# Kernel tuning notes

Hardware: AMD Instinct MI355X
Metric: run time of the kernel (lower is better)

## Reference

```python
import jax, jax.numpy as jnp
import numpy as np

T, B, D, H, L = 512, 512, 64, 128, 2
Y_LEN = 24


def gru_cell(x, h, Wih, Whh, bih, bhh):
    # PyTorch GRU cell, gate order (r, z, n)
    gi = x @ Wih.T + bih          # [B, 3H]
    gh = h @ Whh.T + bhh          # [B, 3H]
    ir, iz, i_n = jnp.split(gi, 3, axis=-1)
    hr, hz, h_n = jnp.split(gh, 3, axis=-1)
    r = jax.nn.sigmoid(ir + hr)
    z = jax.nn.sigmoid(iz + hz)
    n = jnp.tanh(i_n + r * h_n)
    return (1.0 - z) * n + z * h


def bigru_layer(inp, h0, Wih, Whh, bih, bhh):
    # inp [T,B,in]; Wih [2,3H,in]; Whh [2,3H,H]; bih/bhh [2,3H]; h0 [2,B,H]
    def step_f(h, x):
        h = gru_cell(x, h, Wih[0], Whh[0], bih[0], bhh[0])
        return h, h

    def step_b(h, x):
        h = gru_cell(x, h, Wih[1], Whh[1], bih[1], bhh[1])
        return h, h

    hf, out_f = jax.lax.scan(step_f, h0[0], inp)
    hb, out_b = jax.lax.scan(step_b, h0[1], jnp.flip(inp, 0))
    out_b = jnp.flip(out_b, 0)
    return jnp.concatenate([out_f, out_b], -1), hf, hb


def forward(x, enc_Wih0, enc_Wih1, enc_Whh, enc_bih, enc_bhh,
            dec_Wih0, dec_Wih1, dec_Whh, dec_bih, dec_bhh, fc_w, fc_b):
    batch = x.shape[1]
    # ---- encoder: 2-layer bidirectional GRU, h0 = 0 ----
    layer_in = x
    hn = []
    for l in range(L):
        Wih = enc_Wih0 if l == 0 else enc_Wih1
        h0 = jnp.zeros((2, batch, H), x.dtype)
        layer_in, hf, hb = bigru_layer(layer_in, h0, Wih, enc_Whh[l], enc_bih[l], enc_bhh[l])
        hn += [hf, hb]
    dec_h = jnp.stack(hn)                # [2L, B, H], layer-major (fwd, bwd)
    # dropout on h0 is eval-mode identity
    x0 = x[-1, :, 0:1]                   # [B, 1]

    def step(carry, _):
        xin, h = carry
        lin = xin
        new_h = []
        for l in range(L):
            Wih = dec_Wih0 if l == 0 else dec_Wih1
            hf = gru_cell(lin, h[2 * l],     Wih[0], dec_Whh[l, 0], dec_bih[l, 0], dec_bhh[l, 0])
            hb = gru_cell(lin, h[2 * l + 1], Wih[1], dec_Whh[l, 1], dec_bih[l, 1], dec_bhh[l, 1])
            lin = jnp.concatenate([hf, hb], -1)
            new_h += [hf, hb]
        pred = lin @ fc_w.T + fc_b       # [B, 1]
        return (pred, jnp.stack(new_h)), pred[:, 0]

    _, preds = jax.lax.scan(step, (x0, dec_h), None, length=Y_LEN)
    return preds[..., None]              # [24, B, 1]


def setup_inputs():
    key = jax.random.key(0)
    ks = jax.random.split(key, 13)
    scale = 1.0 / np.sqrt(H).astype(np.float32)
    u = lambda k, shape: jax.random.uniform(k, shape, jnp.float32, -scale, scale)
    return {
        "x": jax.random.normal(ks[0], (T, B, D), jnp.float32),
        "enc_Wih0": u(ks[1], (2, 3 * H, D)),
        "enc_Wih1": u(ks[2], (2, 3 * H, 2 * H)),
        "enc_Whh": u(ks[3], (L, 2, 3 * H, H)),
        "enc_bih": u(ks[4], (L, 2, 3 * H)),
        "enc_bhh": u(ks[5], (L, 2, 3 * H)),
        "dec_Wih0": u(ks[6], (2, 3 * H, 1)),
        "dec_Wih1": u(ks[7], (2, 3 * H, 2 * H)),
        "dec_Whh": u(ks[8], (L, 2, 3 * H, H)),
        "dec_bih": u(ks[9], (L, 2, 3 * H)),
        "dec_bhh": u(ks[10], (L, 2, 3 * H)),
        "fc_w": u(ks[11], (1, 2 * H)),
        "fc_b": u(ks[12], (1,)),
    }


def reference(x, enc_Wih0, enc_Wih1, enc_Whh, enc_bih, enc_bhh,
              dec_Wih0, dec_Wih1, dec_Whh, dec_bih, dec_bhh, fc_w, fc_b):
    return forward(x, enc_Wih0, enc_Wih1, enc_Whh, enc_bih, enc_bhh,
                   dec_Wih0, dec_Wih1, dec_Whh, dec_bih, dec_bhh, fc_w, fc_b)
```

## Files before the change

### kernel.cpp

```cpp
#include <hip/hip_runtime.h>
#include <cstdint>
#include <cstddef>


typedef __attribute__((ext_vector_type(8))) short short8_t;
typedef __attribute__((ext_vector_type(4))) short short4_t;
typedef __attribute__((ext_vector_type(4))) float f32x4_t;

#define MFMA16(a, b, c) __builtin_amdgcn_mfma_f32_16x16x32_bf16((a), (b), (c), 0, 0, 0)

static __device__ __forceinline__ float bf2f(unsigned short u) {
  unsigned int v = ((unsigned int)u) << 16;
  return __builtin_bit_cast(float, v);
}
static __device__ __forceinline__ unsigned short f2bf(float f) {
  unsigned int x = __builtin_bit_cast(unsigned int, f);
  x += 0x7fffu + ((x >> 16) & 1u);
  return (unsigned short)(x >> 16);
}
static __device__ __forceinline__ short8_t ld8(const unsigned short* p) {
  return *reinterpret_cast<const short8_t*>(p);
}
static __device__ __forceinline__ short8_t cvt8f(const float* p) {
  const f32x4_t* v = reinterpret_cast<const f32x4_t*>(p);
  f32x4_t a = v[0], b = v[1];
  short8_t r;
  r[0] = (short)f2bf(a[0]); r[1] = (short)f2bf(a[1]);
  r[2] = (short)f2bf(a[2]); r[3] = (short)f2bf(a[3]);
  r[4] = (short)f2bf(b[0]); r[5] = (short)f2bf(b[1]);
  r[6] = (short)f2bf(b[2]); r[7] = (short)f2bf(b[3]);
  return r;
}
static __device__ __forceinline__ float sigm(float x) { return 1.0f / (1.0f + __expf(-x)); }
static __device__ __forceinline__ float tanh_fast(float y) {
  float t = __expf(-2.0f * fabsf(y));
  float r = (1.0f - t) / (1.0f + t);
  return copysignf(r, y);
}

__global__ void k_prep(const float* __restrict__ x,
                       const float* __restrict__ dWih1, const float* __restrict__ dWhh,
                       unsigned short* __restrict__ bdWih1, unsigned short* __restrict__ bdWhh,
                       float* __restrict__ x0save) {
  const int NW = 24576;
  int i = blockIdx.x * blockDim.x + threadIdx.x;
  if (i < NW) {
    *reinterpret_cast<short8_t*>(bdWih1 + (size_t)i * 8) = cvt8f(dWih1 + (size_t)i * 8);
  } else if (i < 2 * NW) {
    int j = i - NW;
    *reinterpret_cast<short8_t*>(bdWhh + (size_t)j * 8) = cvt8f(dWhh + (size_t)j * 8);
  } else if (i < 2 * NW + 512) {
    int b = i - 2 * NW;
    x0save[b] = x[((size_t)511 * 512 + b) * 64];
  }
}

__global__ void k_copy(const float* __restrict__ x, float* __restrict__ xc,
                       int b_base, int Bc) {
  size_t i = (size_t)blockIdx.x * blockDim.x + threadIdx.x;
  size_t per = (size_t)Bc * 16;
  size_t n = (size_t)512 * per;
  if (i >= n) return;
  size_t t = i / per, r = i - t * per;
  const f32x4_t* s =
      reinterpret_cast<const f32x4_t*>(x + ((size_t)t * 512 + b_base) * 64) + r;
  f32x4_t* d = reinterpret_cast<f32x4_t*>(xc + t * per * 4) + r;
  *d = *s;
}

__global__ __launch_bounds__(256, 1) void k_scan0d(
    float* x,
    float* xc,
    const float* __restrict__ Wih,
    const float* __restrict__ bih,
    const float* __restrict__ Whh,
    const float* __restrict__ bhh,
    float* __restrict__ HS,
    int b_base, int Bc) {
  int dir = blockIdx.y;
  int bl0 = blockIdx.x * 16;
  int b0g = b_base + bl0;
  float* xin = dir ? xc : x;
  unsigned short* yout = (unsigned short*)xin;
  int xstr = dir ? Bc : 512;
  int xb0 = dir ? bl0 : b0g;
  int tid = threadIdx.x, w = tid >> 6, lane = tid & 63, q = lane >> 4, c16 = lane & 15;
  __shared__ unsigned short xl[2][16 * 72];
  __shared__ unsigned short hl[2][16 * 136];
  const float* Wi = Wih + (size_t)dir * 384 * 64;
  const float* Wh = Whh + (size_t)dir * 384 * 128;
  const float* bi = bih + dir * 384;
  const float* bh = bhh + dir * 384;

  short8_t fi[6][2], fh[6][4];
  float brz[4], bni[2], bnh[2];
#pragma unroll
  for (int g = 0; g < 3; g++)
#pragma unroll
    for (int cc = 0; cc < 2; cc++) {
      int f = g * 2 + cc;
      int n0 = g * 128 + w * 32 + cc * 16;
#pragma unroll
      for (int kt = 0; kt < 2; kt++)
        fi[f][kt] = cvt8f(Wi + (size_t)(n0 + c16) * 64 + kt * 32 + q * 8);
#pragma unroll
      for (int kt = 0; kt < 4; kt++)
        fh[f][kt] = cvt8f(Wh + (size_t)(n0 + c16) * 128 + kt * 32 + q * 8);
      if (g < 2) brz[f] = bi[n0 + c16] + bh[n0 + c16];
      else { bni[cc] = bi[n0 + c16]; bnh[cc] = bh[n0 + c16]; }
    }

  float h[2][4];
#pragma unroll
  for (int cc = 0; cc < 2; cc++)
#pragma unroll
    for (int rr = 0; rr < 4; rr++) h[cc][rr] = 0.f;
  for (int i = tid; i < 16 * 136; i += 256) hl[0][i] = 0;

  int srow = tid >> 4, sc = tid & 15;
  {
    int t0 = dir ? 511 : 0;
    f32x4_t v = *reinterpret_cast<const f32x4_t*>(
        xin + ((size_t)t0 * xstr + xb0 + srow) * 64 + sc * 4);
    unsigned short* dst = &xl[0][srow * 72 + sc * 4];
    dst[0] = f2bf(v[0]); dst[1] = f2bf(v[1]); dst[2] = f2bf(v[2]); dst[3] = f2bf(v[3]);
  }
  __syncthreads();

  for (int s = 0; s < 512; s++) {
    int cur = s & 1, nxt = cur ^ 1;
    if (s > 0) {
      int tp = dir ? (512 - s) : (s - 1);
      short8_t v = ld8(&hl[cur][srow * 136 + sc * 8]);
      *reinterpret_cast<short8_t*>(
          yout + ((size_t)tp * xstr + xb0 + srow) * 128 + sc * 8) = v;
    }
    f32x4_t xv;
    if (s < 511) {
      int tn = dir ? (510 - s) : (s + 1);
      xv = *reinterpret_cast<const f32x4_t*>(
          xin + ((size_t)tn * xstr + xb0 + srow) * 64 + sc * 4);
    }
    short8_t ax[2], ah[4];
#pragma unroll
    for (int kt = 0; kt < 2; kt++) ax[kt] = ld8(&xl[cur][c16 * 72 + kt * 32 + q * 8]);
#pragma unroll
    for (int kt = 0; kt < 4; kt++) ah[kt] = ld8(&hl[cur][c16 * 136 + kt * 32 + q * 8]);
    f32x4_t aRZ[4], aNi[2], aNh[2];
#pragma unroll
    for (int f = 0; f < 4; f++) aRZ[f] = (f32x4_t){0.f, 0.f, 0.f, 0.f};
#pragma unroll
    for (int cc = 0; cc < 2; cc++) {
      aNi[cc] = (f32x4_t){0.f, 0.f, 0.f, 0.f};
      aNh[cc] = (f32x4_t){0.f, 0.f, 0.f, 0.f};
    }
#pragma unroll
    for (int kt = 0; kt < 2; kt++) {
#pragma unroll
      for (int f = 0; f < 4; f++) aRZ[f] = MFMA16(ax[kt], fi[f][kt], aRZ[f]);
#pragma unroll
      for (int cc = 0; cc < 2; cc++) aNi[cc] = MFMA16(ax[kt], fi[4 + cc][kt], aNi[cc]);
    }
#pragma unroll
    for (int kt = 0; kt < 4; kt++) {
#pragma unroll
      for (int f = 0; f < 4; f++) aRZ[f] = MFMA16(ah[kt], fh[f][kt], aRZ[f]);
#pragma unroll
      for (int cc = 0; cc < 2; cc++) aNh[cc] = MFMA16(ah[kt], fh[4 + cc][kt], aNh[cc]);
    }
#pragma unroll
    for (int cc = 0; cc < 2; cc++)
#pragma unroll
      for (int rr = 0; rr < 4; rr++) {
        float r = sigm(aRZ[cc][rr] + brz[cc]);
        float z = sigm(aRZ[2 + cc][rr] + brz[2 + cc]);
        float n = tanh_fast(aNi[cc][rr] + bni[cc] + r * (aNh[cc][rr] + bnh[cc]));
        float hn = n + z * (h[cc][rr] - n);
        h[cc][rr] = hn;
        hl[nxt][(q * 4 + rr) * 136 + w * 32 + c16 + cc * 16] = f2bf(hn);
      }
    if (s < 511) {
      unsigned short* dst = &xl[nxt][srow * 72 + sc * 4];
      dst[0] = f2bf(xv[0]); dst[1] = f2bf(xv[1]); dst[2] = f2bf(xv[2]); dst[3] = f2bf(xv[3]);
    }
    __syncthreads();
  }
  {
    int tp = dir ? 0 : 511;
    short8_t v = ld8(&hl[0][srow * 136 + sc * 8]);
    *reinterpret_cast<short8_t*>(
        yout + ((size_t)tp * xstr + xb0 + srow) * 128 + sc * 8) = v;
  }
#pragma unroll
  for (int cc = 0; cc < 2; cc++)
#pragma unroll
    for (int rr = 0; rr < 4; rr++)
      HS[((size_t)dir * 512 + b0g + q * 4 + rr) * 128 + w * 32 + c16 + cc * 16] = h[cc][rr];
}

__global__ __launch_bounds__(512, 1) void k_scan1(
    const unsigned short* __restrict__ OutF,
    const unsigned short* __restrict__ OutB,
    const float* __restrict__ Wih1,
    const float* __restrict__ bih1,
    const float* __restrict__ Whh1,
    const float* __restrict__ bhh1,
    float* __restrict__ HS,
    int b_base, int Bc) {
  int dir = blockIdx.y;
  int b0l = blockIdx.x * 16;
  int tid = threadIdx.x, w = tid >> 6, lane = tid & 63, q = lane >> 4, c16 = lane & 15;
  __shared__ unsigned short il[2][16 * 264];
  __shared__ unsigned short hl[2][16 * 136];
  const float* Wi = Wih1 + (size_t)dir * 384 * 256;
  const float* Wh = Whh1 + (size_t)dir * 384 * 128;
  const float* bi = bih1 + dir * 384;
  const float* bh = bhh1 + dir * 384;

  short8_t fi[3][8], fh[3][4];
  float brz[2], bni, bnh;
#pragma unroll
  for (int g = 0; g < 3; g++) {
    int n0 = g * 128 + w * 16;
#pragma unroll
    for (int kt = 0; kt < 8; kt++)
      fi[g][kt] = cvt8f(Wi + (size_t)(n0 + c16) * 256 + kt * 32 + q * 8);
#pragma unroll
    for (int kt = 0; kt < 4; kt++)
      fh[g][kt] = cvt8f(Wh + (size_t)(n0 + c16) * 128 + kt * 32 + q * 8);
    if (g < 2) brz[g] = bi[n0 + c16] + bh[n0 + c16];
    else { bni = bi[n0 + c16]; bnh = bh[n0 + c16]; }
  }

  float h[4] = {0.f, 0.f, 0.f, 0.f};
  for (int i = tid; i < 16 * 136; i += 512) hl[0][i] = 0;

  int srow = tid >> 5, sc = tid & 31;
  {
    int t0 = dir ? 511 : 0;
    short8_t v = (sc < 16)
        ? ld8(OutF + ((size_t)t0 * 512 + b_base + b0l + srow) * 128 + sc * 8)
        : ld8(OutB + ((size_t)t0 * Bc + b0l + srow) * 128 + (sc - 16) * 8);
    *reinterpret_cast<short8_t*>(&il[0][srow * 264 + sc * 8]) = v;
  }
  __syncthreads();

  for (int s = 0; s < 512; s++) {
    int cur = s & 1, nxt = cur ^ 1;
    short8_t iv;
    if (s < 511) {
      int tn = dir ? (510 - s) : (s + 1);
      iv = (sc < 16)
          ? ld8(OutF + ((size_t)tn * 512 + b_base + b0l + srow) * 128 + sc * 8)
          : ld8(OutB + ((size_t)tn * Bc + b0l + srow) * 128 + (sc - 16) * 8);
    }
    f32x4_t aI[3], aH[3];
#pragma unroll
    for (int g = 0; g < 3; g++) {
      aI[g] = (f32x4_t){0.f, 0.f, 0.f, 0.f};
      aH[g] = (f32x4_t){0.f, 0.f, 0.f, 0.f};
    }
#pragma unroll
    for (int kt = 0; kt < 8; kt++) {
      short8_t a = ld8(&il[cur][c16 * 264 + kt * 32 + q * 8]);
#pragma unroll
      for (int g = 0; g < 3; g++) aI[g] = MFMA16(a, fi[g][kt], aI[g]);
    }
#pragma unroll
    for (int kt = 0; kt < 4; kt++) {
      short8_t a = ld8(&hl[cur][c16 * 136 + kt * 32 + q * 8]);
#pragma unroll
      for (int g = 0; g < 3; g++) aH[g] = MFMA16(a, fh[g][kt], aH[g]);
    }
#pragma unroll
    for (int rr = 0; rr < 4; rr++) {
      float r = sigm(aI[0][rr] + aH[0][rr] + brz[0]);
      float z = sigm(aI[1][rr] + aH[1][rr] + brz[1]);
      float n = tanh_fast(aI[2][rr] + bni + r * (aH[2][rr] + bnh));
      float hn = n + z * (h[rr] - n);
      h[rr] = hn;
      hl[nxt][(q * 4 + rr) * 136 + w * 16 + c16] = f2bf(hn);
    }
    if (s < 511)
      *reinterpret_cast<short8_t*>(&il[nxt][srow * 264 + sc * 8]) = iv;
    __syncthreads();
  }
#pragma unroll
  for (int rr = 0; rr < 4; rr++)
    HS[((size_t)(2 + dir) * 512 + b_base + b0l + q * 4 + rr) * 128 + w * 16 + c16] = h[rr];
}

__global__ __launch_bounds__(512, 1) void k_dec(
    const float* __restrict__ x0save,
    const float* __restrict__ HS,
    const unsigned short* __restrict__ Whh,
    const unsigned short* __restrict__ Wih1,
    const float* __restrict__ Wih0,
    const float* __restrict__ bih,
    const float* __restrict__ bhh,
    const float* __restrict__ fc_w,
    const float* __restrict__ fcb,
    float* __restrict__ out) {
  int b0 = blockIdx.x * 16;
  int tid = threadIdx.x, w = tid >> 6, lane = tid & 63, q = lane >> 4, c16 = lane & 15;
  int d = w >> 2, w4 = w & 3;
  __shared__ unsigned short hc0[16 * 264];
  __shared__ unsigned short hc1[16 * 264];
  __shared__ float x0s[16];
  __shared__ float fcwf[256];
  int jj = w4 * 32 + c16;
  int jw = w4 * 32;

  const unsigned short* Wd0 = Whh + (size_t)d * 384 * 128;
  const unsigned short* Wh1 = Whh + (size_t)(2 + d) * 384 * 128;
  const unsigned short* Wi1 = Wih1 + (size_t)d * 384 * 256;

  float hs[2][2][4];
#pragma unroll
  for (int l = 0; l < 2; l++)
#pragma unroll
    for (int cc = 0; cc < 2; cc++)
#pragma unroll
      for (int rr = 0; rr < 4; rr++) {
        int row = q * 4 + rr, j = jj + cc * 16;
        int cell = l * 2 + d;
        float v = HS[((size_t)cell * 512 + b0 + row) * 128 + j];
        hs[l][cc][rr] = v;
        unsigned short bv = f2bf(v);
        unsigned short* tile = l ? hc1 : hc0;
        tile[row * 264 + d * 128 + j] = bv;
      }
  if (tid < 16) x0s[tid] = x0save[b0 + tid];
  if (tid < 256) fcwf[tid] = fc_w[tid];

  float w0c[2][3], bi0[2][3], bh0[2][3], bi1[2][3], bh1[2][3];
#pragma unroll
  for (int cc = 0; cc < 2; cc++)
#pragma unroll
    for (int g = 0; g < 3; g++) {
      int col = g * 128 + jj + cc * 16;
      w0c[cc][g] = Wih0[d * 384 + col];
      bi0[cc][g] = bih[d * 384 + col];
      bh0[cc][g] = bhh[d * 384 + col];
      bi1[cc][g] = bih[(2 + d) * 384 + col];
      bh1[cc][g] = bhh[(2 + d) * 384 + col];
    }
  __syncthreads();

  for (int st = 0; st < 24; st++) {
    float hn0[2][4];
    {
      short8_t a0[4];
#pragma unroll
      for (int kt = 0; kt < 4; kt++)
        a0[kt] = ld8(&hc0[c16 * 264 + d * 128 + kt * 32 + q * 8]);
      short8_t w0[24];
#pragma unroll
      for (int kt = 0; kt < 4; kt++)
#pragma unroll
        for (int g = 0; g < 3; g++)
#pragma unroll
          for (int cc = 0; cc < 2; cc++) {
            int n0 = g * 128 + jw + cc * 16;
            w0[kt * 6 + g * 2 + cc] =
                ld8(Wd0 + (size_t)(n0 + c16) * 128 + kt * 32 + q * 8);
          }
      f32x4_t acc[6];
#pragma unroll
      for (int f = 0; f < 6; f++) acc[f] = (f32x4_t){0.f, 0.f, 0.f, 0.f};
#pragma unroll
      for (int kt = 0; kt < 4; kt++)
#pragma unroll
        for (int g = 0; g < 3; g++)
#pragma unroll
          for (int cc = 0; cc < 2; cc++) {
            int f = g * 2 + cc;
            acc[f] = MFMA16(a0[kt], w0[kt * 6 + g * 2 + cc], acc[f]);
          }
#pragma unroll
      for (int cc = 0; cc < 2; cc++)
#pragma unroll
        for (int rr = 0; rr < 4; rr++) {
          float xin = x0s[q * 4 + rr];
          float r = sigm(xin * w0c[cc][0] + bi0[cc][0] + acc[cc][rr] + bh0[cc][0]);
          float z = sigm(xin * w0c[cc][1] + bi0[cc][1] + acc[2 + cc][rr] + bh0[cc][1]);
          float n = tanh_fast(xin * w0c[cc][2] + bi0[cc][2] +
                              r * (acc[4 + cc][rr] + bh0[cc][2]));
          float hv = n + z * (hs[0][cc][rr] - n);
          hn0[cc][rr] = hv;
          hs[0][cc][rr] = hv;
        }
    }
    __syncthreads();
#pragma unroll
    for (int cc = 0; cc < 2; cc++)
#pragma unroll
      for (int rr = 0; rr < 4; rr++)
        hc0[(q * 4 + rr) * 264 + d * 128 + jj + cc * 16] = f2bf(hn0[cc][rr]);
    __syncthreads();

    float hn1[2][4];
    {
      short8_t ai[8];
#pragma unroll
      for (int kt = 0; kt < 8; kt++) ai[kt] = ld8(&hc0[c16 * 264 + kt * 32 + q * 8]);
      short8_t ah[4];
#pragma unroll
      for (int kt = 0; kt < 4; kt++)
        ah[kt] = ld8(&hc1[c16 * 264 + d * 128 + kt * 32 + q * 8]);
      f32x4_t aRZ[4], aNi[2], aNh[2];
#pragma unroll
      for (int f = 0; f < 4; f++) aRZ[f] = (f32x4_t){0.f, 0.f, 0.f, 0.f};
#pragma unroll
      for (int cc = 0; cc < 2; cc++) {
        aNi[cc] = (f32x4_t){0.f, 0.f, 0.f, 0.f};
        aNh[cc] = (f32x4_t){0.f, 0.f, 0.f, 0.f};
      }
      {
        short8_t wA[24];
#pragma unroll
        for (int kt = 0; kt < 4; kt++) {
#pragma unroll
          for (int f = 0; f < 4; f++) {
            int n0 = (f >> 1) * 128 + jw + (f & 1) * 16;
            wA[kt * 6 + f] = ld8(Wi1 + (size_t)(n0 + c16) * 256 + kt * 32 + q * 8);
          }
#pragma unroll
          for (int cc = 0; cc < 2; cc++) {
            int n0 = 256 + jw + cc * 16;
            wA[kt * 6 + 4 + cc] = ld8(Wi1 + (size_t)(n0 + c16) * 256 + kt * 32 + q * 8);
          }
        }
#pragma unroll
        for (int kt = 0; kt < 4; kt++) {
#pragma unroll
          for (int f = 0; f < 4; f++) aRZ[f] = MFMA16(ai[kt], wA[kt * 6 + f], aRZ[f]);
#pragma unroll
          for (int cc = 0; cc < 2; cc++) aNi[cc] = MFMA16(ai[kt], wA[kt * 6 + 4 + cc], aNi[cc]);
        }
      }
      {
        short8_t wB[24];
#pragma unroll
        for (int kt = 0; kt < 4; kt++) {
#pragma unroll
          for (int f = 0; f < 4; f++) {
            int n0 = (f >> 1) * 128 + jw + (f & 1) * 16;
            wB[kt * 6 + f] = ld8(Wi1 + (size_t)(n0 + c16) * 256 + (kt + 4) * 32 + q * 8);
          }
#pragma unroll
          for (int cc = 0; cc < 2; cc++) {
            int n0 = 256 + jw + cc * 16;
            wB[kt * 6 + 4 + cc] = ld8(Wi1 + (size_t)(n0 + c16) * 256 + (kt + 4) * 32 + q * 8);
          }
        }
#pragma unroll
        for (int kt = 0; kt < 4; kt++) {
#pragma unroll
          for (int f = 0; f < 4; f++) aRZ[f] = MFMA16(ai[4 + kt], wB[kt * 6 + f], aRZ[f]);
#pragma unroll
          for (int cc = 0; cc < 2; cc++) aNi[cc] = MFMA16(ai[4 + kt], wB[kt * 6 + 4 + cc], aNi[cc]);
        }
      }
      {
        short8_t wH[24];
#pragma unroll
        for (int kt = 0; kt < 4; kt++) {
#pragma unroll
          for (int f = 0; f < 4; f++) {
            int n0 = (f >> 1) * 128 + jw + (f & 1) * 16;
            wH[kt * 6 + f] = ld8(Wh1 + (size_t)(n0 + c16) * 128 + kt * 32 + q * 8);
          }
#pragma unroll
          for (int cc = 0; cc < 2; cc++) {
            int n0 = 256 + jw + cc * 16;
            wH[kt * 6 + 4 + cc] = ld8(Wh1 + (size_t)(n0 + c16) * 128 + kt * 32 + q * 8);
          }
        }
#pragma unroll
        for (int kt = 0; kt < 4; kt++) {
#pragma unroll
          for (int f = 0; f < 4; f++) aRZ[f] = MFMA16(ah[kt], wH[kt * 6 + f], aRZ[f]);
#pragma unroll
          for (int cc = 0; cc < 2; cc++) aNh[cc] = MFMA16(ah[kt], wH[kt * 6 + 4 + cc], aNh[cc]);
        }
      }
#pragma unroll
      for (int cc = 0; cc < 2; cc++)
#pragma unroll
        for (int rr = 0; rr < 4; rr++) {
          float r = sigm(aRZ[cc][rr] + bi1[cc][0] + bh1[cc][0]);
          float z = sigm(aRZ[2 + cc][rr] + bi1[cc][1] + bh1[cc][1]);
          float n = tanh_fast(aNi[cc][rr] + bi1[cc][2] + r * (aNh[cc][rr] + bh1[cc][2]));
          float hv = n + z * (hs[1][cc][rr] - n);
          hn1[cc][rr] = hv;
          hs[1][cc][rr] = hv;
        }
    }
    __syncthreads();
#pragma unroll
    for (int cc = 0; cc < 2; cc++)
#pragma unroll
      for (int rr = 0; rr < 4; rr++)
        hc1[(q * 4 + rr) * 264 + d * 128 + jj + cc * 16] = f2bf(hn1[cc][rr]);
    __syncthreads();

    if (w == 0) {
      float s = 0.f;
#pragma unroll
      for (int i = 0; i < 8; i++) {
        short8_t hv = ld8(&hc1[c16 * 264 + q * 64 + i * 8]);
#pragma unroll
        for (int e = 0; e < 8; e++)
          s += bf2f((unsigned short)hv[e]) * fcwf[q * 64 + i * 8 + e];
      }
      s += __shfl_xor(s, 16);
      s += __shfl_xor(s, 32);
      if (q == 0) {
        float pred = s + fcb[0];
        x0s[c16] = pred;
        out[(size_t)st * 512 + b0 + c16] = pred;
      }
    }
    __syncthreads();
  }
}

extern "C" void kernel_launch(void* const* d_in, const int* in_sizes, int n_in,
                              void* d_out, int out_size, void* d_ws, size_t ws_size,
                              hipStream_t stream) {
  const float* x     = (const float*)d_in[0];
  const float* eWih0 = (const float*)d_in[1];
  const float* eWih1 = (const float*)d_in[2];
  const float* eWhh  = (const float*)d_in[3];
  const float* ebih  = (const float*)d_in[4];
  const float* ebhh  = (const float*)d_in[5];
  const float* dWih0 = (const float*)d_in[6];
  const float* dWih1 = (const float*)d_in[7];
  const float* dWhh  = (const float*)d_in[8];
  const float* dbih  = (const float*)d_in[9];
  const float* dbhh  = (const float*)d_in[10];
  const float* fc_w  = (const float*)d_in[11];
  const float* fc_b  = (const float*)d_in[12];
  float* out = (float*)d_out;
  (void)in_sizes; (void)n_in; (void)out_size;

  const size_t fixedB = 2048 + 1048576 + 393216 + 393216 + 4096;
  int Bc = 256;
  if (fixedB + (size_t)512 * 131072 <= ws_size) Bc = 512;

  char* ws = (char*)d_ws;
  size_t off = 0;
  auto alloc = [&](size_t bytes) -> char* {
    off = (off + 255) & ~(size_t)255;
    char* p = ws + off;
    off += bytes;
    return p;
  };
  float* x0save          = (float*)alloc(2048);
  float* HS              = (float*)alloc(1048576);
  unsigned short* bdWih1 = (unsigned short*)alloc(393216);
  unsigned short* bdWhh  = (unsigned short*)alloc(393216);
  float* xc              = (float*)alloc((size_t)Bc * 131072);

  k_prep<<<194, 256, 0, stream>>>(x, dWih1, dWhh, bdWih1, bdWhh, x0save);

  float* xm = (float*)d_in[0];
  const float* Whh1 = eWhh + (size_t)2 * 384 * 128;
  int nchunks = 512 / Bc;
  for (int c = 0; c < nchunks; c++) {
    int b_base = c * Bc;
    int ncopy = (512 * Bc * 16 + 255) / 256;
    k_copy<<<ncopy, 256, 0, stream>>>(x, xc, b_base, Bc);
    k_scan0d<<<dim3(Bc / 16, 2), 256, 0, stream>>>(xm, xc, eWih0, ebih, eWhh, ebhh,
                                                   HS, b_base, Bc);
    k_scan1<<<dim3(Bc / 16, 2), 512, 0, stream>>>((const unsigned short*)xm,
                                                  (const unsigned short*)xc,
                                                  eWih1, ebih + 768, Whh1,
                                                  ebhh + 768, HS, b_base, Bc);
  }
  k_dec<<<dim3(32), 512, 0, stream>>>(x0save, HS, bdWhh, bdWih1, dWih0, dbih, dbhh,
                                      fc_w, fc_b, out);
}
```

Measured before the change: 2.083 ms.

## Prefetch scan inputs two steps ahead and use LDS-only barrier

Both encoder scan kernels now issue the global load for the input two timesteps ahead, keeping it in registers that alternate between two buffers via a manually unrolled loop of two steps. The per-step __syncthreads is replaced with an inline-asm barrier that waits only on LDS counters, so the outstanding global prefetch no longer has to finish at each barrier. This is meant to hide global load latency on the serial recurrence critical path. The cost is extra registers, plus reliance on the asm barrier being correct for the ordering of the global y-output stores.

```diff
diff --git a/kernel.cpp b/kernel.cpp
--- a/kernel.cpp
+++ b/kernel.cpp
@@ -8,6 +8,8 @@
 typedef __attribute__((ext_vector_type(4))) float f32x4_t;
 
 #define MFMA16(a, b, c) __builtin_amdgcn_mfma_f32_16x16x32_bf16((a), (b), (c), 0, 0, 0)
+
+#define BAR_LDS() asm volatile("s_waitcnt lgkmcnt(0)\n\ts_barrier" ::: "memory")
 
 static __device__ __forceinline__ float bf2f(unsigned short u) {
   unsigned int v = ((unsigned int)u) << 16;
@@ -20,6 +22,9 @@
 }
 static __device__ __forceinline__ short8_t ld8(const unsigned short* p) {
   return *reinterpret_cast<const short8_t*>(p);
+}
+static __device__ __forceinline__ f32x4_t ldf4(const float* p) {
+  return *reinterpret_cast<const f32x4_t*>(p);
 }
 static __device__ __forceinline__ short8_t cvt8f(const float* p) {
   const f32x4_t* v = reinterpret_cast<const f32x4_t*>(p);
@@ -120,26 +125,28 @@
   int srow = tid >> 4, sc = tid & 15;
   {
     int t0 = dir ? 511 : 0;
-    f32x4_t v = *reinterpret_cast<const f32x4_t*>(
-        xin + ((size_t)t0 * xstr + xb0 + srow) * 64 + sc * 4);
+    f32x4_t v = ldf4(xin + ((size_t)t0 * xstr + xb0 + srow) * 64 + sc * 4);
     unsigned short* dst = &xl[0][srow * 72 + sc * 4];
     dst[0] = f2bf(v[0]); dst[1] = f2bf(v[1]); dst[2] = f2bf(v[2]); dst[3] = f2bf(v[3]);
   }
+  f32x4_t pA, pB;
+  {
+    int t1 = dir ? 510 : 1;
+    pA = ldf4(xin + ((size_t)t1 * xstr + xb0 + srow) * 64 + sc * 4);
+  }
   __syncthreads();
 
-  for (int s = 0; s < 512; s++) {
+  auto body = [&](int s, const f32x4_t& xu, f32x4_t& xnl) {
     int cur = s & 1, nxt = cur ^ 1;
+    if (s < 510) {
+      int tn = dir ? (509 - s) : (s + 2);
+      xnl = ldf4(xin + ((size_t)tn * xstr + xb0 + srow) * 64 + sc * 4);
+    }
     if (s > 0) {
       int tp = dir ? (512 - s) : (s - 1);
       short8_t v = ld8(&hl[cur][srow * 136 + sc * 8]);
       *reinterpret_cast<short8_t*>(
           yout + ((size_t)tp * xstr + xb0 + srow) * 128 + sc * 8) = v;
-    }
-    f32x4_t xv;
-    if (s < 511) {
-      int tn = dir ? (510 - s) : (s + 1);
-      xv = *reinterpret_cast<const f32x4_t*>(
-          xin + ((size_t)tn * xstr + xb0 + srow) * 64 + sc * 4);
     }
     short8_t ax[2], ah[4];
 #pragma unroll
@@ -181,9 +188,14 @@
       }
     if (s < 511) {
       unsigned short* dst = &xl[nxt][srow * 72 + sc * 4];
-      dst[0] = f2bf(xv[0]); dst[1] = f2bf(xv[1]); dst[2] = f2bf(xv[2]); dst[3] = f2bf(xv[3]);
-    }
-    __syncthreads();
+      dst[0] = f2bf(xu[0]); dst[1] = f2bf(xu[1]); dst[2] = f2bf(xu[2]); dst[3] = f2bf(xu[3]);
+    }
+    BAR_LDS();
+  };
+
+  for (int s2 = 0; s2 < 256; s2++) {
+    body(2 * s2, pA, pB);
+    body(2 * s2 + 1, pB, pA);
   }
   {
     int tp = dir ? 0 : 511;
@@ -243,14 +255,20 @@
         : ld8(OutB + ((size_t)t0 * Bc + b0l + srow) * 128 + (sc - 16) * 8);
     *reinterpret_cast<short8_t*>(&il[0][srow * 264 + sc * 8]) = v;
   }
+  short8_t ivA, ivB;
+  {
+    int t1 = dir ? 510 : 1;
+    ivA = (sc < 16)
+        ? ld8(OutF + ((size_t)t1 * 512 + b_base + b0l + srow) * 128 + sc * 8)
+        : ld8(OutB + ((size_t)t1 * Bc + b0l + srow) * 128 + (sc - 16) * 8);
+  }
   __syncthreads();
 
-  for (int s = 0; s < 512; s++) {
+  auto body = [&](int s, const short8_t& iu, short8_t& inl) {
     int cur = s & 1, nxt = cur ^ 1;
-    short8_t iv;
-    if (s < 511) {
-      int tn = dir ? (510 - s) : (s + 1);
-      iv = (sc < 16)
+    if (s < 510) {
+      int tn = dir ? (509 - s) : (s + 2);
+      inl = (sc < 16)
           ? ld8(OutF + ((size_t)tn * 512 + b_base + b0l + srow) * 128 + sc * 8)
           : ld8(OutB + ((size_t)tn * Bc + b0l + srow) * 128 + (sc - 16) * 8);
     }
@@ -282,8 +300,13 @@
       hl[nxt][(q * 4 + rr) * 136 + w * 16 + c16] = f2bf(hn);
     }
     if (s < 511)
-      *reinterpret_cast<short8_t*>(&il[nxt][srow * 264 + sc * 8]) = iv;
-    __syncthreads();
+      *reinterpret_cast<short8_t*>(&il[nxt][srow * 264 + sc * 8]) = iu;
+    BAR_LDS();
+  };
+
+  for (int s2 = 0; s2 < 256; s2++) {
+    body(2 * s2, ivA, ivB);
+    body(2 * s2 + 1, ivB, ivA);
   }
 #pragma unroll
   for (int rr = 0; rr < 4; rr++)
```

Result: no change. 2.057 ms (-1.2%).
